# Optimization experiments

Hardware: AMD Instinct MI355X
Metric: run time of the kernel (lower is better)

Reference implementation:

```python
import jax, jax.numpy as jnp
import numpy as np

PATCH_NUMS = (1, 2, 3, 4, 5, 6, 8, 10, 13, 16)
B = 8
NUM_HEADS = 24
HEAD_DIM = 64
C = NUM_HEADS * HEAD_DIM  # 1536
ROPE_BASE = 10000.0


def _position_ids(batch):
    # Mirrors get_position_ids: 2D grid coords per scale, rescaled to the largest grid.
    largest = PATCH_NUMS[-1]
    coords = []
    for pn in PATCH_NUMS:
        g = np.stack(np.meshgrid(np.arange(pn), np.arange(pn), indexing='ij'), axis=-1)
        coords.append((g.astype(np.float64) / pn * largest).reshape(-1, 2))
    pos = np.concatenate(coords, axis=0).astype(np.float32)  # [L, 2]
    return jnp.asarray(np.broadcast_to(pos, (batch,) + pos.shape))


def setup_inputs() -> dict:
    key = jax.random.key(0)
    k0, k1, k2 = jax.random.split(key, 3)
    L = sum(p * p for p in PATCH_NUMS)  # 680
    s = 0.02
    return {
        'x': jax.random.normal(k0, (B, L, C), jnp.float32),
        'pos_ids': _position_ids(B),                                   # [B, L, 2] float coords
        'w_qkv': jax.random.normal(k1, (3 * C, C), jnp.float32) * s,   # fused QKV weight (no bias in Linear)
        'q_bias': jnp.zeros((C,), jnp.float32),                        # learnable q bias
        'v_bias': jnp.zeros((C,), jnp.float32),                        # learnable v bias (k bias is fixed zero)
        'w_o': jax.random.normal(k2, (C, C), jnp.float32) * s,
        'b_o': jnp.zeros((C,), jnp.float32),
    }


def _rope_2d_cos_sin(pos_ids):
    # LlamaRotaryEmbedding (2D): inv_freq over head_dim with step 4; each spatial axis
    # gets head_dim/2 rotary channels laid out as [fx, fx, fy, fy] (rotate-half pairing).
    inv_freq = 1.0 / (ROPE_BASE ** (jnp.arange(0, HEAD_DIM, 4, dtype=jnp.float32) / HEAD_DIM))  # [hd/4]
    f = pos_ids[..., None] * inv_freq                      # [B, L, 2, hd/4]
    f2 = jnp.concatenate([f, f], axis=-1)                  # [B, L, 2, hd/2]
    emb = f2.reshape(f2.shape[0], f2.shape[1], HEAD_DIM)   # [B, L, hd]
    return jnp.cos(emb), jnp.sin(emb)


def _rotate_half(t):
    h = t.shape[-1] // 2
    return jnp.concatenate([-t[..., h:], t[..., :h]], axis=-1)


def reference(x, pos_ids, w_qkv, q_bias, v_bias, w_o, b_o):
    Bb, L, Cc = x.shape
    bias = jnp.concatenate([q_bias, jnp.zeros_like(q_bias), v_bias])  # zero k bias
    qkv = (x @ w_qkv.T + bias).reshape(Bb, L, 3, NUM_HEADS, HEAD_DIM)
    q, k, v = qkv[:, :, 0], qkv[:, :, 1], qkv[:, :, 2]  # bshd

    cos, sin = _rope_2d_cos_sin(pos_ids)                # [B, L, hd]
    cos = cos[:, :, None, :]                            # broadcast over heads (unsqueeze_dim=2)
    sin = sin[:, :, None, :]
    q = q * cos + _rotate_half(q) * sin
    k = k * cos + _rotate_half(k) * sin

    scale = 1.0 / jnp.sqrt(jnp.asarray(HEAD_DIM, jnp.float32))
    scores = jnp.einsum('bshd,bthd->bhst', q, k) * scale  # [B, H, L, L]
    attn = jax.nn.softmax(scores, axis=-1)
    out = jnp.einsum('bhst,bthd->bshd', attn, v).reshape(Bb, L, Cc)
    return out @ w_o.T + b_o
```

## Files before the change

### kernel.cpp

```cpp
#include <hip/hip_runtime.h>
#include <cmath>

typedef _Float16 f16;
typedef _Float16 f16x2 __attribute__((ext_vector_type(2)));
typedef _Float16 f16x4 __attribute__((ext_vector_type(4)));
typedef _Float16 f16x8 __attribute__((ext_vector_type(8)));
typedef float f32x4 __attribute__((ext_vector_type(4)));

namespace {

constexpr int kB = 8;
constexpr int kL = 680;
constexpr int kH = 24;
constexpr int kD = 64;
constexpr int kC = 1536;
constexpr int kM = kB * kL;
constexpr int kN3 = 3 * kC;
constexpr int kNKT = 11;
constexpr int kNQT = 6;

#define ASYNC_CP16(gp, lp)                                          \
  __builtin_amdgcn_global_load_lds(                                 \
      (const __attribute__((address_space(1))) unsigned int*)(gp),  \
      (__attribute__((address_space(3))) unsigned int*)(lp), 16, 0, 0)

__device__ inline int xcd_swizzle(int bid, int nwg) {
  int q = nwg >> 3, r = nwg & 7;
  int x = bid & 7, idx = bid >> 3;
  return (x < r ? x * (q + 1) : r * (q + 1) + (x - r) * q) + idx;
}

__device__ inline void stripe_decode(int id, int gx, int gy, int& mt,
                                     int& nt) {
  const int SW = 4;
  int nst = (gx + SW - 1) / SW;
  int s = id / (gy * SW);
  if (s > nst - 1) s = nst - 1;
  int rem = id - s * gy * SW;
  int w = gx - s * SW;
  if (w > SW) w = SW;
  mt = rem / w;
  nt = s * SW + rem % w;
}

__global__ void cvt_f32_f16(const float* __restrict__ in,
                            f16* __restrict__ out, int n) {
  int i = (blockIdx.x * blockDim.x + threadIdx.x) * 4;
  if (i >= n) return;
  float4 v = *reinterpret_cast<const float4*>(&in[i]);
  f16x4 o;
  o[0] = (f16)v.x;
  o[1] = (f16)v.y;
  o[2] = (f16)v.z;
  o[3] = (f16)v.w;
  *reinterpret_cast<f16x4*>(&out[i]) = o;
}

__global__ void build_bias_kernel(const float* __restrict__ qb,
                                  const float* __restrict__ vb,
                                  float* __restrict__ bias) {
  int i = blockIdx.x * blockDim.x + threadIdx.x;
  if (i >= kN3) return;
  float v = 0.0f;
  if (i < kC) v = qb[i];
  else if (i >= 2 * kC) v = vb[i - 2 * kC];
  bias[i] = v;
}

template <typename OutT, bool ROPE>
__global__ __launch_bounds__(512, 2) void gemm256_8ph(
    const f16* __restrict__ A, const f16* __restrict__ Bw,
    const float* __restrict__ bias, OutT* __restrict__ Cm,
    const float* __restrict__ pos, int M, int N, int K) {
  constexpr int HALF = 8192;
  constexpr int ABUF = 2 * HALF;
  constexpr int BUF = 2 * ABUF;
  __shared__ __align__(16) f16 sm[2 * BUF];

  const int tid = threadIdx.x;
  const int w = tid >> 6;
  const int lane = tid & 63;
  const int lr = lane & 15;
  const int quad = lane >> 4;
  const int wr = w >> 2;
  const int wc = w & 3;
  const int gx = gridDim.x;
  const int sw = xcd_swizzle(blockIdx.y * gx + blockIdx.x, gx * gridDim.y);
  int mt, nt;
  stripe_decode(sw, gx, gridDim.y, mt, nt);
  const int m0 = mt * 256;
  const int n0 = nt * 256;
  const int NT = K >> 6;

  const f16* aptr[2][2];
  const f16* bptr[2][2];
  int dstoff0 = tid * 8;
  int dstoff1 = (tid + 512) * 8;
#pragma unroll
  for (int h = 0; h < 2; ++h) {
#pragma unroll
    for (int n = 0; n < 2; ++n) {
      int idx = n * 512 + tid;
      int kb = idx >> 7, r = idx & 127;
      int ra = m0 + h * 128 + r;
      if (ra > M - 1) ra = M - 1;
      aptr[h][n] = A + (size_t)ra * K + kb * 8;
      bptr[h][n] = Bw + (size_t)(n0 + h * 128 + r) * K + kb * 8;
    }
  }

  auto stageA = [&](int t, int h, int q) {
    f16* d = &sm[q * BUF + h * HALF];
    ASYNC_CP16(aptr[h][0] + t * 64, &d[dstoff0]);
    ASYNC_CP16(aptr[h][1] + t * 64, &d[dstoff1]);
  };
  auto stageB = [&](int t, int h, int q) {
    f16* d = &sm[q * BUF + ABUF + h * HALF];
    ASYNC_CP16(bptr[h][0] + t * 64, &d[dstoff0]);
    ASYNC_CP16(bptr[h][1] + t * 64, &d[dstoff1]);
  };

  f32x4 acc[8][4];
#pragma unroll
  for (int i = 0; i < 8; ++i)
#pragma unroll
    for (int j = 0; j < 4; ++j)
#pragma unroll
      for (int c = 0; c < 4; ++c) acc[i][j][c] = 0.0f;

  const int bRow0 = (wc & 1) * 64;

  stageA(0, 0, 0);
  stageA(0, 1, 0);
  stageB(0, 0, 0);
  stageB(0, 1, 0);
  stageB(1, 0, 1);
  stageB(1, 1, 1);
  asm volatile("s_waitcnt vmcnt(4)" ::: "memory");
  __builtin_amdgcn_s_barrier();

  const int NIT = NT >> 1;
  for (int itr = 0; itr < NIT; ++itr) {
    const int t0 = itr * 2;
#pragma unroll
    for (int hf = 0; hf < 2; ++hf) {
      const int tcur = t0 + hf;
      const int ta = tcur + 1;
      const int tb = tcur + 2;
      const f16* Aq = &sm[hf * BUF + wr * HALF];
      const f16* Bq = &sm[hf * BUF + ABUF + (wc >> 1) * HALF];
      f16x8 a0[4], a1[4], b0[4], b1[4];

#pragma unroll
      for (int i = 0; i < 4; ++i)
        a0[i] = *reinterpret_cast<const f16x8*>(
            &Aq[((quad << 7) + i * 16 + lr) * 8]);
#pragma unroll
      for (int j = 0; j < 4; ++j)
        b0[j] = *reinterpret_cast<const f16x8*>(
            &Bq[((quad << 7) + bRow0 + j * 16 + lr) * 8]);
      if (ta < NT) stageA(ta, 0, hf ^ 1);
      __builtin_amdgcn_s_barrier();
      asm volatile("s_waitcnt lgkmcnt(0)" ::: "memory");
      __builtin_amdgcn_s_setprio(1);
#pragma unroll
      for (int i = 0; i < 4; ++i)
#pragma unroll
        for (int j = 0; j < 4; ++j)
          acc[i][j] = __builtin_amdgcn_mfma_f32_16x16x32_f16(
              a0[i], b0[j], acc[i][j], 0, 0, 0);
      __builtin_amdgcn_s_setprio(0);
      __builtin_amdgcn_s_barrier();

#pragma unroll
      for (int j = 0; j < 4; ++j)
        b1[j] = *reinterpret_cast<const f16x8*>(
            &Bq[(((4 + quad) << 7) + bRow0 + j * 16 + lr) * 8]);
#pragma unroll
      for (int i = 0; i < 4; ++i)
        a1[i] = *reinterpret_cast<const f16x8*>(
            &Aq[((quad << 7) + (i + 4) * 16 + lr) * 8]);
      if (ta < NT) stageA(ta, 1, hf ^ 1);
      __builtin_amdgcn_s_barrier();
      asm volatile("s_waitcnt lgkmcnt(0)" ::: "memory");
      __builtin_amdgcn_s_setprio(1);
#pragma unroll
      for (int i = 0; i < 4; ++i)
#pragma unroll
        for (int j = 0; j < 4; ++j)
          acc[i + 4][j] = __builtin_amdgcn_mfma_f32_16x16x32_f16(
              a1[i], b0[j], acc[i + 4][j], 0, 0, 0);
      __builtin_amdgcn_s_setprio(0);
      __builtin_amdgcn_s_barrier();

#pragma unroll
      for (int i = 0; i < 4; ++i)
        a0[i] = *reinterpret_cast<const f16x8*>(
            &Aq[(((4 + quad) << 7) + i * 16 + lr) * 8]);
      if (tb < NT) stageB(tb, 0, hf);
      __builtin_amdgcn_s_barrier();
      asm volatile("s_waitcnt lgkmcnt(0)" ::: "memory");
      __builtin_amdgcn_s_setprio(1);
#pragma unroll
      for (int i = 0; i < 4; ++i)
#pragma unroll
        for (int j = 0; j < 4; ++j)
          acc[i][j] = __builtin_amdgcn_mfma_f32_16x16x32_f16(
              a0[i], b1[j], acc[i][j], 0, 0, 0);
      __builtin_amdgcn_s_setprio(0);
      __builtin_amdgcn_s_barrier();

#pragma unroll
      for (int i = 0; i < 4; ++i)
        a1[i] = *reinterpret_cast<const f16x8*>(
            &Aq[(((4 + quad) << 7) + (i + 4) * 16 + lr) * 8]);
      if (tb < NT) stageB(tb, 1, hf);
      __builtin_amdgcn_s_barrier();
      asm volatile("s_waitcnt lgkmcnt(0)" ::: "memory");
      __builtin_amdgcn_s_setprio(1);
#pragma unroll
      for (int i = 0; i < 4; ++i)
#pragma unroll
        for (int j = 0; j < 4; ++j)
          acc[i + 4][j] = __builtin_amdgcn_mfma_f32_16x16x32_f16(
              a1[i], b1[j], acc[i + 4][j], 0, 0, 0);
      __builtin_amdgcn_s_setprio(0);
      if (tb < NT)
        asm volatile("s_waitcnt vmcnt(4)" ::: "memory");
      else
        asm volatile("s_waitcnt vmcnt(0)" ::: "memory");
      __builtin_amdgcn_s_barrier();
    }
  }

  float bv[4];
#pragma unroll
  for (int j = 0; j < 4; ++j) bv[j] = bias[n0 + wc * 64 + j * 16 + lr];

  if (ROPE && n0 < 2 * kC) {
    const float fr = exp2f(-(float)lr * (13.287712379549449f / 16.0f));
#pragma unroll
    for (int i = 0; i < 8; ++i) {
#pragma unroll
      for (int r = 0; r < 4; ++r) {
        int row = m0 + wr * 128 + i * 16 + quad * 4 + r;
        if (row < M) {
          float a0r = pos[row * 2 + 0] * fr;
          float a1r = pos[row * 2 + 1] * fr;
          float s0 = __sinf(a0r), c0 = __cosf(a0r);
          float s1 = __sinf(a1r), c1 = __cosf(a1r);
#pragma unroll
          for (int j = 0; j < 2; ++j) {
            float v0 = acc[i][j][r] + bv[j];
            float v1 = acc[i][j + 2][r] + bv[j + 2];
            int col = n0 + wc * 64 + j * 16 + lr;
            Cm[(size_t)row * N + col] = (OutT)(v0 * c0 - v1 * s0);
            Cm[(size_t)row * N + col + 32] = (OutT)(v1 * c1 + v0 * s1);
          }
        }
      }
    }
  } else {
#pragma unroll
    for (int i = 0; i < 8; ++i) {
#pragma unroll
      for (int j = 0; j < 4; ++j) {
#pragma unroll
        for (int r = 0; r < 4; ++r) {
          int row = m0 + wr * 128 + i * 16 + quad * 4 + r;
          if (row < M) {
            int col = n0 + wc * 64 + j * 16 + lr;
            Cm[(size_t)row * N + col] = (OutT)(acc[i][j][r] + bv[j]);
          }
        }
      }
    }
  }
}

__global__ __launch_bounds__(256, 3) void attn_mfma(
    const f16* __restrict__ qkv, f16* __restrict__ attnout) {
  __shared__ __align__(16) f16 Ks[64 * 72];
  __shared__ __align__(16) f16 Vts[64 * 72];
  __shared__ __align__(16) f16 Pl[4][32 * 72];

  const int tid = threadIdx.x;
  const int w = tid >> 6;
  const int lane = tid & 63;
  const int lr = lane & 15;
  const int qd = lane >> 4;

  const int bid = blockIdx.x;
  const int xcd = bid & 7;
  const int rest = bid >> 3;
  const int qt = rest % kNQT;
  const int g = xcd + 8 * (rest / kNQT);
  const int h = g % kH;
  const int b = g / kH;
  const int q0 = qt * 128;

  f16x8 aq[2][2];
#pragma unroll
  for (int rt = 0; rt < 2; ++rt) {
    int qrow = q0 + w * 32 + rt * 16 + lr;
    if (qrow > kL - 1) qrow = kL - 1;
    const f16* qp = qkv + (size_t)(b * kL + qrow) * kN3 + h * kD;
#pragma unroll
    for (int ks = 0; ks < 2; ++ks)
      aq[rt][ks] =
          *reinterpret_cast<const f16x8*>(qp + ks * 32 + qd * 8);
  }

  const int kkey0 = tid >> 3, kdc = tid & 7;
  const int kkey1 = (tid + 256) >> 3;
  const int vkey0 = (tid & 31) * 2;
  const int vd0 = (tid >> 5) * 8;

  f16x8 kpre0, kpre1, vpre0, vpre1;
  auto prefetch = [&](int kt0) {
    int kg0 = kt0 + kkey0;
    if (kg0 > kL - 1) kg0 = kL - 1;
    kpre0 = *reinterpret_cast<const f16x8*>(
        qkv + (size_t)(b * kL + kg0) * kN3 + kC + h * kD + kdc * 8);
    int kg1 = kt0 + kkey1;
    if (kg1 > kL - 1) kg1 = kL - 1;
    kpre1 = *reinterpret_cast<const f16x8*>(
        qkv + (size_t)(b * kL + kg1) * kN3 + kC + h * kD + kdc * 8);
    int vg0 = kt0 + vkey0;
    if (vg0 > kL - 1) vg0 = kL - 1;
    vpre0 = *reinterpret_cast<const f16x8*>(
        qkv + (size_t)(b * kL + vg0) * kN3 + 2 * kC + h * kD + vd0);
    int vg1 = kt0 + vkey0 + 1;
    if (vg1 > kL - 1) vg1 = kL - 1;
    vpre1 = *reinterpret_cast<const f16x8*>(
        qkv + (size_t)(b * kL + vg1) * kN3 + 2 * kC + h * kD + vd0);
  };
  prefetch(0);

  f32x4 o_acc[2][4];
#pragma unroll
  for (int rt = 0; rt < 2; ++rt)
#pragma unroll
    for (int nt = 0; nt < 4; ++nt)
#pragma unroll
      for (int r = 0; r < 4; ++r) o_acc[rt][nt][r] = 0.0f;
  float lsum[2][4] = {{0.f, 0.f, 0.f, 0.f}, {0.f, 0.f, 0.f, 0.f}};

  for (int it = 0; it < kNKT; ++it) {
    const int kt0 = it * 64;
    __syncthreads();

    *reinterpret_cast<f16x8*>(&Ks[kkey0 * 72 + kdc * 8]) = kpre0;
    *reinterpret_cast<f16x8*>(&Ks[kkey1 * 72 + kdc * 8]) = kpre1;
#pragma unroll
    for (int i = 0; i < 8; ++i) {
      f16x2 pr;
      pr[0] = vpre0[i];
      pr[1] = vpre1[i];
      *reinterpret_cast<f16x2*>(&Vts[(vd0 + i) * 72 + vkey0]) = pr;
    }
    prefetch((it < kNKT - 1) ? (it + 1) * 64 : it * 64);
    __syncthreads();

    f32x4 s_acc[2][4];
#pragma unroll
    for (int rt = 0; rt < 2; ++rt)
#pragma unroll
      for (int t = 0; t < 4; ++t)
#pragma unroll
        for (int r = 0; r < 4; ++r) s_acc[rt][t][r] = 0.0f;
#pragma unroll
    for (int ks = 0; ks < 2; ++ks) {
#pragma unroll
      for (int t = 0; t < 4; ++t) {
        f16x8 bk = *reinterpret_cast<const f16x8*>(
            &Ks[(t * 16 + lr) * 72 + ks * 32 + qd * 8]);
        s_acc[0][t] = __builtin_amdgcn_mfma_f32_16x16x32_f16(
            aq[0][ks], bk, s_acc[0][t], 0, 0, 0);
        s_acc[1][t] = __builtin_amdgcn_mfma_f32_16x16x32_f16(
            aq[1][ks], bk, s_acc[1][t], 0, 0, 0);
      }
    }

#pragma unroll
    for (int rt = 0; rt < 2; ++rt) {
#pragma unroll
      for (int t = 0; t < 4; ++t) {
        const bool valid = (kt0 + t * 16 + lr) < kL;
#pragma unroll
        for (int r = 0; r < 4; ++r) {
          float p = valid ? __expf(s_acc[rt][t][r] * 0.125f) : 0.0f;
          lsum[rt][r] += p;
          Pl[w][(rt * 16 + qd * 4 + r) * 72 + t * 16 + lr] = (f16)p;
        }
      }
    }

#pragma unroll
    for (int ks = 0; ks < 2; ++ks) {
      f16x8 ap[2];
#pragma unroll
      for (int rt = 0; rt < 2; ++rt)
        ap[rt] = *reinterpret_cast<const f16x8*>(
            &Pl[w][(rt * 16 + lr) * 72 + ks * 32 + qd * 8]);
#pragma unroll
      for (int nt = 0; nt < 4; ++nt) {
        f16x8 bv = *reinterpret_cast<const f16x8*>(
            &Vts[(nt * 16 + lr) * 72 + ks * 32 + qd * 8]);
        o_acc[0][nt] = __builtin_amdgcn_mfma_f32_16x16x32_f16(
            ap[0], bv, o_acc[0][nt], 0, 0, 0);
        o_acc[1][nt] = __builtin_amdgcn_mfma_f32_16x16x32_f16(
            ap[1], bv, o_acc[1][nt], 0, 0, 0);
      }
    }
  }

#pragma unroll
  for (int rt = 0; rt < 2; ++rt)
#pragma unroll
    for (int r = 0; r < 4; ++r) {
#pragma unroll
      for (int m = 1; m < 16; m <<= 1)
        lsum[rt][r] += __shfl_xor(lsum[rt][r], m, 64);
    }

#pragma unroll
  for (int rt = 0; rt < 2; ++rt) {
#pragma unroll
    for (int nt = 0; nt < 4; ++nt) {
#pragma unroll
      for (int r = 0; r < 4; ++r) {
        int qr = q0 + w * 32 + rt * 16 + qd * 4 + r;
        if (qr < kL) {
          attnout[(size_t)(b * kL + qr) * kC + h * kD + nt * 16 + lr] =
              (f16)(o_acc[rt][nt][r] / lsum[rt][r]);
        }
      }
    }
  }
}

}

extern "C" void kernel_launch(void* const* d_in, const int* in_sizes, int n_in,
                              void* d_out, int out_size, void* d_ws,
                              size_t ws_size, hipStream_t stream) {
  const float* x = (const float*)d_in[0];
  const float* pos = (const float*)d_in[1];
  const float* w_qkv = (const float*)d_in[2];
  const float* q_bias = (const float*)d_in[3];
  const float* v_bias = (const float*)d_in[4];
  const float* w_o = (const float*)d_in[5];
  const float* b_o = (const float*)d_in[6];
  float* out = (float*)d_out;

  f16* qkv16 = (f16*)d_ws;
  f16* x16 = qkv16 + (size_t)kM * kN3;
  f16* wqkv16 = x16 + (size_t)kM * kC;
  f16* wo16 = wqkv16 + (size_t)kN3 * kC;
  f16* ao16 = wo16 + (size_t)kC * kC;
  float* bias_full = (float*)(ao16 + (size_t)kM * kC);

  cvt_f32_f16<<<(kM * kC / 4 + 255) / 256, 256, 0, stream>>>(x, x16, kM * kC);
  cvt_f32_f16<<<(kN3 * kC / 4 + 255) / 256, 256, 0, stream>>>(w_qkv, wqkv16,
                                                              kN3 * kC);
  cvt_f32_f16<<<(kC * kC / 4 + 255) / 256, 256, 0, stream>>>(w_o, wo16,
                                                             kC * kC);
  build_bias_kernel<<<(kN3 + 255) / 256, 256, 0, stream>>>(q_bias, v_bias,
                                                           bias_full);
  gemm256_8ph<f16, true><<<dim3(kN3 / 256, (kM + 255) / 256), 512, 0,
                           stream>>>(x16, wqkv16, bias_full, qkv16, pos, kM,
                                     kN3, kC);
  attn_mfma<<<dim3(kNQT * kH * kB), 256, 0, stream>>>(qkv16, ao16);
  gemm256_8ph<float, false><<<dim3(kC / 256, (kM + 255) / 256), 512, 0,
                              stream>>>(ao16, wo16, b_o, out, nullptr, kM, kC,
                                        kC);
}
```

Baseline: 377.8 us.

## Split-K the output projection GEMM and fuse conversion kernels into one launch

The four conversion and bias-building kernels become a single launch that dispatches on a flat chunk index. The output projection GEMM now runs split-K with a z-dimension of 2, the second half writing fp32 partials into the workspace, followed by a reduce_add kernel. This doubles the block count of the small 6x22-tile projection grid to fill more compute units, at the cost of an extra 33MB of partial read/write traffic and one more launch. The partial buffer reuses the start of the workspace (qkv16), which is safe only because attention has already consumed it.

Result: slower. 406.0 us (+7.5%).

```diff
diff --git a/kernel.cpp b/kernel.cpp
--- a/kernel.cpp
+++ b/kernel.cpp
@@ -43,35 +43,65 @@
   nt = s * SW + rem % w;
 }
 
-__global__ void cvt_f32_f16(const float* __restrict__ in,
-                            f16* __restrict__ out, int n) {
-  int i = (blockIdx.x * blockDim.x + threadIdx.x) * 4;
-  if (i >= n) return;
-  float4 v = *reinterpret_cast<const float4*>(&in[i]);
+__global__ void fused_cvt_bias(const float* __restrict__ x,
+                               const float* __restrict__ wqkv,
+                               const float* __restrict__ wo,
+                               const float* __restrict__ qb,
+                               const float* __restrict__ vb,
+                               f16* __restrict__ x16,
+                               f16* __restrict__ wqkv16,
+                               f16* __restrict__ wo16,
+                               float* __restrict__ bias) {
+  const int c0 = kM * kC / 4, c1 = kN3 * kC / 4, c2 = kC * kC / 4,
+            c3 = kN3 / 4;
+  int i = blockIdx.x * blockDim.x + threadIdx.x;
+  const float* src = nullptr;
+  f16* dst = nullptr;
+  if (i < c0) {
+    src = x; dst = x16;
+  } else if ((i -= c0) < c1) {
+    src = wqkv; dst = wqkv16;
+  } else if ((i -= c1) < c2) {
+    src = wo; dst = wo16;
+  } else if ((i -= c2) < c3) {
+    int base = i * 4;
+    float vv[4];
+#pragma unroll
+    for (int k2 = 0; k2 < 4; ++k2) {
+      int idx = base + k2;
+      float b = 0.0f;
+      if (idx < kC) b = qb[idx];
+      else if (idx >= 2 * kC) b = vb[idx - 2 * kC];
+      vv[k2] = b;
+    }
+    *reinterpret_cast<float4*>(&bias[base]) =
+        make_float4(vv[0], vv[1], vv[2], vv[3]);
+    return;
+  } else {
+    return;
+  }
+  float4 v = *reinterpret_cast<const float4*>(&src[i * 4]);
   f16x4 o;
-  o[0] = (f16)v.x;
-  o[1] = (f16)v.y;
-  o[2] = (f16)v.z;
-  o[3] = (f16)v.w;
-  *reinterpret_cast<f16x4*>(&out[i]) = o;
-}
-
-__global__ void build_bias_kernel(const float* __restrict__ qb,
-                                  const float* __restrict__ vb,
-                                  float* __restrict__ bias) {
+  o[0] = (f16)v.x; o[1] = (f16)v.y; o[2] = (f16)v.z; o[3] = (f16)v.w;
+  *reinterpret_cast<f16x4*>(&dst[i * 4]) = o;
+}
+
+__global__ void reduce_add(float* __restrict__ out,
+                           const float* __restrict__ part, int n4) {
   int i = blockIdx.x * blockDim.x + threadIdx.x;
-  if (i >= kN3) return;
-  float v = 0.0f;
-  if (i < kC) v = qb[i];
-  else if (i >= 2 * kC) v = vb[i - 2 * kC];
-  bias[i] = v;
+  if (i >= n4) return;
+  float4 a = *reinterpret_cast<const float4*>(&out[i * 4]);
+  float4 b = *reinterpret_cast<const float4*>(&part[i * 4]);
+  a.x += b.x; a.y += b.y; a.z += b.z; a.w += b.w;
+  *reinterpret_cast<float4*>(&out[i * 4]) = a;
 }
 
 template <typename OutT, bool ROPE>
 __global__ __launch_bounds__(512, 2) void gemm256_8ph(
     const f16* __restrict__ A, const f16* __restrict__ Bw,
-    const float* __restrict__ bias, OutT* __restrict__ Cm,
-    const float* __restrict__ pos, int M, int N, int K) {
+    const float* __restrict__ bias0, OutT* __restrict__ Cm0,
+    OutT* __restrict__ Cm1, const float* __restrict__ pos, int M, int N,
+    int K, int tHalf) {
   constexpr int HALF = 8192;
   constexpr int ABUF = 2 * HALF;
   constexpr int BUF = 2 * ABUF;
@@ -90,7 +120,21 @@
   stripe_decode(sw, gx, gridDim.y, mt, nt);
   const int m0 = mt * 256;
   const int n0 = nt * 256;
-  const int NT = K >> 6;
+
+  const int NTall = K >> 6;
+  int tS = 0, tE = NTall;
+  OutT* Cm = Cm0;
+  const float* bias = bias0;
+  if (gridDim.z == 2) {
+    if (blockIdx.z == 1) {
+      tS = tHalf;
+      Cm = Cm1;
+      bias = nullptr;
+    } else {
+      tE = tHalf;
+    }
+  }
+  const int NTt = tE - tS;
 
   const f16* aptr[2][2];
   const f16* bptr[2][2];
@@ -130,21 +174,21 @@
 
   const int bRow0 = (wc & 1) * 64;
 
-  stageA(0, 0, 0);
-  stageA(0, 1, 0);
-  stageB(0, 0, 0);
-  stageB(0, 1, 0);
-  stageB(1, 0, 1);
-  stageB(1, 1, 1);
+  stageA(tS, 0, 0);
+  stageA(tS, 1, 0);
+  stageB(tS, 0, 0);
+  stageB(tS, 1, 0);
+  stageB(tS + 1, 0, 1);
+  stageB(tS + 1, 1, 1);
   asm volatile("s_waitcnt vmcnt(4)" ::: "memory");
   __builtin_amdgcn_s_barrier();
 
-  const int NIT = NT >> 1;
+  const int NIT = NTt >> 1;
   for (int itr = 0; itr < NIT; ++itr) {
-    const int t0 = itr * 2;
+    const int tt0 = itr * 2;
 #pragma unroll
     for (int hf = 0; hf < 2; ++hf) {
-      const int tcur = t0 + hf;
+      const int tcur = tS + tt0 + hf;
       const int ta = tcur + 1;
       const int tb = tcur + 2;
       const f16* Aq = &sm[hf * BUF + wr * HALF];
@@ -159,7 +203,7 @@
       for (int j = 0; j < 4; ++j)
         b0[j] = *reinterpret_cast<const f16x8*>(
             &Bq[((quad << 7) + bRow0 + j * 16 + lr) * 8]);
-      if (ta < NT) stageA(ta, 0, hf ^ 1);
+      if (ta < tE) stageA(ta, 0, hf ^ 1);
       __builtin_amdgcn_s_barrier();
       asm volatile("s_waitcnt lgkmcnt(0)" ::: "memory");
       __builtin_amdgcn_s_setprio(1);
@@ -180,7 +224,7 @@
       for (int i = 0; i < 4; ++i)
         a1[i] = *reinterpret_cast<const f16x8*>(
             &Aq[((quad << 7) + (i + 4) * 16 + lr) * 8]);
-      if (ta < NT) stageA(ta, 1, hf ^ 1);
+      if (ta < tE) stageA(ta, 1, hf ^ 1);
       __builtin_amdgcn_s_barrier();
       asm volatile("s_waitcnt lgkmcnt(0)" ::: "memory");
       __builtin_amdgcn_s_setprio(1);
@@ -197,7 +241,7 @@
       for (int i = 0; i < 4; ++i)
         a0[i] = *reinterpret_cast<const f16x8*>(
             &Aq[(((4 + quad) << 7) + i * 16 + lr) * 8]);
-      if (tb < NT) stageB(tb, 0, hf);
+      if (tb < tE) stageB(tb, 0, hf);
       __builtin_amdgcn_s_barrier();
       asm volatile("s_waitcnt lgkmcnt(0)" ::: "memory");
       __builtin_amdgcn_s_setprio(1);
@@ -214,7 +258,7 @@
       for (int i = 0; i < 4; ++i)
         a1[i] = *reinterpret_cast<const f16x8*>(
             &Aq[(((4 + quad) << 7) + (i + 4) * 16 + lr) * 8]);
-      if (tb < NT) stageB(tb, 1, hf);
+      if (tb < tE) stageB(tb, 1, hf);
       __builtin_amdgcn_s_barrier();
       asm volatile("s_waitcnt lgkmcnt(0)" ::: "memory");
       __builtin_amdgcn_s_setprio(1);
@@ -225,7 +269,7 @@
           acc[i + 4][j] = __builtin_amdgcn_mfma_f32_16x16x32_f16(
               a1[i], b1[j], acc[i + 4][j], 0, 0, 0);
       __builtin_amdgcn_s_setprio(0);
-      if (tb < NT)
+      if (tb < tE)
         asm volatile("s_waitcnt vmcnt(4)" ::: "memory");
       else
         asm volatile("s_waitcnt vmcnt(0)" ::: "memory");
@@ -235,7 +279,8 @@
 
   float bv[4];
 #pragma unroll
-  for (int j = 0; j < 4; ++j) bv[j] = bias[n0 + wc * 64 + j * 16 + lr];
+  for (int j = 0; j < 4; ++j)
+    bv[j] = bias ? bias[n0 + wc * 64 + j * 16 + lr] : 0.0f;
 
   if (ROPE && n0 < 2 * kC) {
     const float fr = exp2f(-(float)lr * (13.287712379549449f / 16.0f));
@@ -460,19 +505,22 @@
   f16* wo16 = wqkv16 + (size_t)kN3 * kC;
   f16* ao16 = wo16 + (size_t)kC * kC;
   float* bias_full = (float*)(ao16 + (size_t)kM * kC);
-
-  cvt_f32_f16<<<(kM * kC / 4 + 255) / 256, 256, 0, stream>>>(x, x16, kM * kC);
-  cvt_f32_f16<<<(kN3 * kC / 4 + 255) / 256, 256, 0, stream>>>(w_qkv, wqkv16,
-                                                              kN3 * kC);
-  cvt_f32_f16<<<(kC * kC / 4 + 255) / 256, 256, 0, stream>>>(w_o, wo16,
-                                                             kC * kC);
-  build_bias_kernel<<<(kN3 + 255) / 256, 256, 0, stream>>>(q_bias, v_bias,
-                                                           bias_full);
-  gemm256_8ph<f16, true><<<dim3(kN3 / 256, (kM + 255) / 256), 512, 0,
-                           stream>>>(x16, wqkv16, bias_full, qkv16, pos, kM,
-                                     kN3, kC);
+  float* proj_part = (float*)d_ws;
+
+  {
+    const int c0 = kM * kC / 4, c1 = kN3 * kC / 4, c2 = kC * kC / 4,
+              c3 = kN3 / 4;
+    int nchunks = c0 + c1 + c2 + c3;
+    fused_cvt_bias<<<(nchunks + 255) / 256, 256, 0, stream>>>(
+        x, w_qkv, w_o, q_bias, v_bias, x16, wqkv16, wo16, bias_full);
+  }
+  gemm256_8ph<f16, true><<<dim3(kN3 / 256, (kM + 255) / 256, 1), 512, 0,
+                           stream>>>(x16, wqkv16, bias_full, qkv16, nullptr,
+                                     pos, kM, kN3, kC, 0);
   attn_mfma<<<dim3(kNQT * kH * kB), 256, 0, stream>>>(qkv16, ao16);
-  gemm256_8ph<float, false><<<dim3(kC / 256, (kM + 255) / 256), 512, 0,
-                              stream>>>(ao16, wo16, b_o, out, nullptr, kM, kC,
-                                        kC);
-}
+  gemm256_8ph<float, false><<<dim3(kC / 256, (kM + 255) / 256, 2), 512, 0,
+                              stream>>>(ao16, wo16, b_o, out, proj_part,
+                                        nullptr, kM, kC, kC, 12);
+  reduce_add<<<(kM * kC / 4 + 255) / 256, 256, 0, stream>>>(out, proj_part,
+                                                            kM * kC / 4);
+}
```
